# Kernel optimization log

Hardware: AMD Instinct MI355X
Metric: run time of the kernel (lower is better)

The kernel has to match this reference:

```python
import jax, jax.numpy as jnp
import numpy as np

KS = 3
PAD = 1
N = KS * KS  # 9 sampling points


def setup_inputs() -> dict:
    key = jax.random.key(0)
    k1, k2, k3 = jax.random.split(key, 3)
    B, C, H, W = 8, 64, 96, 96
    OUT = 64
    x = jax.random.normal(k1, (B, C, H, W), jnp.float32)
    offset = jax.random.normal(k2, (B, 2 * N, H, W), jnp.float32)
    conv_w = jax.random.normal(k3, (OUT, C * N, KS, KS), jnp.float32) * 0.02
    conv_b = jnp.zeros((OUT,), jnp.float32)
    return {"x": x, "offset": offset, "conv_w": conv_w, "conv_b": conv_b}


def _deform_gather(x, offset):
    # zero-pad spatially (nn.ZeroPad2d)
    xp = jnp.pad(x, ((0, 0), (0, 0), (PAD, PAD), (PAD, PAD)))
    b, c, h, w = xp.shape
    _, _, ho, wo = offset.shape
    # base kernel grid (row, col) pairs, shape (N, 2)
    grid = jnp.stack(
        jnp.meshgrid(jnp.arange(KS), jnp.arange(KS), indexing='ij'), axis=-1
    ).reshape(-1, 2).astype(offset.dtype)
    # offsets: (b, 2N, ho, wo) -> (b, ho, wo, N, 2)
    off = offset.transpose(0, 2, 3, 1).reshape(b, ho, wo, N, 2)
    p = grid[None, None, None] + off                       # (b, ho, wo, N, 2)
    # replicate torch's non-contiguous permute+reshape exactly (row-major)
    p = p.transpose(0, 3, 1, 2, 4).reshape(b, 2 * N, ho, wo)
    qx = jnp.clip(p[:, :N], 0, w - 1)                      # (b, N, ho, wo)
    qy = jnp.clip(p[:, N:], 0, h - 1)
    x0 = jnp.clip(jnp.floor(qx).astype(jnp.int32), 0, w - 1)
    x1 = jnp.clip(x0 + 1, 0, w - 1)
    y0 = jnp.clip(jnp.floor(qy).astype(jnp.int32), 0, h - 1)
    y1 = jnp.clip(y0 + 1, 0, h - 1)
    xf = xp.reshape(b, c, h * w)

    def g(iy, ix):
        idx = (iy * w + ix).reshape(b, 1, -1)              # (b, 1, N*ho*wo)
        v = jnp.take_along_axis(
            xf, jnp.broadcast_to(idx, (b, c, idx.shape[-1])), axis=2)
        return v.reshape(b, c, N, ho, wo)

    v00 = g(y0, x0); v01 = g(y0, x1); v10 = g(y1, x0); v11 = g(y1, x1)
    wx = (qx - x0.astype(qx.dtype))[:, None]               # (b, 1, N, ho, wo)
    wy = (qy - y0.astype(qy.dtype))[:, None]
    val = (v00 * (1 - wx) + v01 * wx) * (1 - wy) + (v10 * (1 - wx) + v11 * wx) * wy
    # (b, c, N, ho, wo) -> (b, c, ho, wo, N) -> (b, c*N, ho, wo)
    return val.transpose(0, 1, 3, 4, 2).reshape(b, c * N, ho, wo)


def reference(x, offset, conv_w, conv_b):
    xo = _deform_gather(x, offset)
    out = jax.lax.conv_general_dilated(
        xo, conv_w, window_strides=(1, 1), padding='VALID',
        dimension_numbers=('NCHW', 'OIHW', 'NCHW'))
    return out + conv_b[None, :, None, None]
```

## Files before the change

kernel.cpp:

```cpp
#include <hip/hip_runtime.h>

typedef short bf16x8 __attribute__((ext_vector_type(8)));
typedef float f32x4  __attribute__((ext_vector_type(4)));
typedef float f32x16 __attribute__((ext_vector_type(16)));

#define Sx 9216
#define ROWW 96
#define WB_USHORTS 331776
#define OW 94
#define XO_USHORTS ((size_t)8 * 96 * ROWW * 576)
#define XT_OFF_BYTES (2 * (size_t)WB_USHORTS + 2 * XO_USHORTS)
#define NEED_NEW (XT_OFF_BYTES + (size_t)8 * Sx * 64 * 4)
#define NOUT 4524032

__device__ __forceinline__ unsigned short bf16r(float f) {
    unsigned int u = __float_as_uint(f);
    u += 0x7fffu + ((u >> 16) & 1u);
    return (unsigned short)(u >> 16);
}

__device__ __forceinline__ void gload16(const void* g, void* l) {
    __builtin_amdgcn_global_load_lds(
        (const __attribute__((address_space(1))) void*)g,
        (__attribute__((address_space(3))) void*)l, 16, 0, 0);
}

__global__ __launch_bounds__(256)
void wprep32_k(const float* __restrict__ w, unsigned short* __restrict__ Wb) {
    int id = blockIdx.x * 256 + threadIdx.x;
    if (id >= 648 * 64) return;
    int lane = id & 63;
    int fm   = id >> 6;
    int m    = fm & 1;
    int rest = fm >> 1;
    int k16  = rest & 3;
    int rest2= rest >> 2;
    int qc   = rest2 / 9;
    int t    = rest2 - qc * 9;
    int o    = m * 32 + (lane & 31);
    int cb   = k16 * 16 + (lane >> 5) * 8;
    unsigned short v[8];
    #pragma unroll
    for (int j = 0; j < 8; ++j)
        v[j] = bf16r(w[(size_t)o * 5184 + ((cb + j) * 9 + qc) * 9 + t]);
    uint4 u;
    u.x = v[0] | ((unsigned)v[1] << 16);
    u.y = v[2] | ((unsigned)v[3] << 16);
    u.z = v[4] | ((unsigned)v[5] << 16);
    u.w = v[6] | ((unsigned)v[7] << 16);
    *(uint4*)(Wb + (size_t)id * 8) = u;
}

__global__ __launch_bounds__(256)
void wprep_k(const float* __restrict__ w, unsigned short* __restrict__ Wb) {
    int id = blockIdx.x * 256 + threadIdx.x;
    if (id >= 162 * 4 * 64) return;
    int lane = id & 63;
    int fm   = id >> 6;
    int mt   = fm & 3;
    int step = fm >> 2;
    int qc   = step / 18;
    int rs   = step - qc * 18;
    int t    = rs >> 1;
    int q32  = rs & 1;
    int o    = mt * 16 + (lane & 15);
    int cib  = q32 * 32 + (lane >> 4) * 8;
    unsigned short v[8];
    #pragma unroll
    for (int j = 0; j < 8; ++j) {
        int qorig = (cib + j) * 9 + qc;
        v[j] = bf16r(w[(size_t)o * 5184 + qorig * 9 + t]);
    }
    uint4 u;
    u.x = v[0] | ((unsigned)v[1] << 16);
    u.y = v[2] | ((unsigned)v[3] << 16);
    u.z = v[4] | ((unsigned)v[5] << 16);
    u.w = v[6] | ((unsigned)v[7] << 16);
    *(uint4*)(Wb + (size_t)id * 8) = u;
}

__global__ __launch_bounds__(256)
void xt_k(const float* __restrict__ x, float* __restrict__ xt) {
    __shared__ float t[64][65];
    const int tid = threadIdx.x;
    const int r2b = blockIdx.x * 64;
    const int b   = blockIdx.y;
    const int qq  = tid >> 6;
    const int ll  = tid & 63;
    #pragma unroll
    for (int cc = 0; cc < 16; ++cc) {
        int ci = cc * 4 + qq;
        t[ci][ll] = x[((size_t)(b * 64 + ci)) * Sx + r2b + ll];
    }
    __syncthreads();
    #pragma unroll
    for (int rr = 0; rr < 16; ++rr) {
        int r2l = rr * 4 + qq;
        xt[((size_t)b * Sx + r2b + r2l) * 64 + ll] = t[ll][r2l];
    }
}

__device__ __forceinline__ void decode_phase1(
        const float* __restrict__ ob, int x0b, int y,
        int (*sA)[288], float (*sW)[288], int tid) {
    for (int e = tid; e < 288; e += 256) {
        int chr = e >> 5;
        int xl  = e & 31;
        int r2  = y * 96 + x0b + xl;
        int n   = r2 % 9;
        int r   = chr * 1024 + r2 / 9;
        float q2[2];
        #pragma unroll
        for (int c2 = 0; c2 < 2; ++c2) {
            int k    = n + 9 * c2;
            int f    = k * Sx + r;
            int nn   = f / 18432;
            int t    = f - nn * 18432;
            int comp = t & 1;
            int pos  = t >> 1;
            int nd3  = nn / 3;
            float gg = comp ? (float)(nn - nd3 * 3) : (float)nd3;
            q2[c2] = gg + ob[(size_t)(2 * nn + comp) * Sx + pos];
        }
        float qx = fminf(fmaxf(q2[0], 0.f), 97.f);
        float qy = fminf(fmaxf(q2[1], 0.f), 97.f);
        int x0 = (int)qx; if (x0 > 97) x0 = 97;
        int y0 = (int)qy; if (y0 > 97) y0 = 97;
        float fx = qx - (float)x0;
        float fy = qy - (float)y0;
        int x1 = x0 + 1; if (x1 > 97) x1 = 97;
        int y1 = y0 + 1; if (y1 > 97) y1 = 97;
        int ix0 = x0 - 1, ix1 = x1 - 1, iy0 = y0 - 1, iy1 = y1 - 1;
        float vx0 = (ix0 >= 0 && ix0 < 96) ? 1.f : 0.f;
        float vx1 = (ix1 >= 0 && ix1 < 96) ? 1.f : 0.f;
        float vy0 = (iy0 >= 0 && iy0 < 96) ? 1.f : 0.f;
        float vy1 = (iy1 >= 0 && iy1 < 96) ? 1.f : 0.f;
        int cx0 = min(max(ix0, 0), 95), cx1 = min(max(ix1, 0), 95);
        int cy0 = min(max(iy0, 0), 95), cy1 = min(max(iy1, 0), 95);
        sW[0][e] = (1.f - fx) * (1.f - fy) * vx0 * vy0;
        sW[1][e] = fx * (1.f - fy) * vx1 * vy0;
        sW[2][e] = (1.f - fx) * fy * vx0 * vy1;
        sW[3][e] = fx * fy * vx1 * vy1;
        sA[0][e] = cy0 * 96 + cx0;
        sA[1][e] = cy0 * 96 + cx1;
        sA[2][e] = cy1 * 96 + cx0;
        sA[3][e] = cy1 * 96 + cx1;
    }
}

__global__ __launch_bounds__(256, 4)
void gather_xt(const float* __restrict__ xt, const float* __restrict__ off,
               unsigned short* __restrict__ xo) {
    __shared__ int   sA[4][288];
    __shared__ float sW[4][288];
    const int tid = threadIdx.x;
    const int x0b = blockIdx.x * 32;
    const int y   = blockIdx.y;
    const int b   = blockIdx.z;
    decode_phase1(off + (size_t)b * 18 * Sx, x0b, y, sA, sW, tid);
    __syncthreads();

    const int lane = tid & 63;
    const int wv   = tid >> 6;
    const float* xtb = xt + (size_t)b * Sx * 64 + lane;
    unsigned short* xob =
        xo + ((size_t)(b * 96 + y) * ROWW + x0b) * 576 + lane;

    #pragma unroll 4
    for (int i = 0; i < 72; ++i) {
        int e   = wv * 72 + i;
        int chr = e >> 5;
        int xl  = e & 31;
        float v = sW[0][e] * xtb[(size_t)sA[0][e] * 64]
                + sW[1][e] * xtb[(size_t)sA[1][e] * 64]
                + sW[2][e] * xtb[(size_t)sA[2][e] * 64]
                + sW[3][e] * xtb[(size_t)sA[3][e] * 64];
        xob[xl * 576 + chr * 64] = bf16r(v);
    }
}

__global__ __launch_bounds__(256, 2)
void gather_fb(const float* __restrict__ x, const float* __restrict__ off,
               unsigned short* __restrict__ xo) {
    __shared__ int   sA[4][288];
    __shared__ float sW[4][288];
    const int tid = threadIdx.x;
    const int x0b = blockIdx.x * 32;
    const int y   = blockIdx.y;
    const int b   = blockIdx.z;
    decode_phase1(off + (size_t)b * 18 * Sx, x0b, y, sA, sW, tid);
    __syncthreads();

    const int xl = tid & 31;
    const int g  = tid >> 5;
    const float* xb = x + (size_t)b * 64 * Sx + (size_t)g * 8 * Sx;
    uint4* dst = (uint4*)(xo + ((size_t)(b * 96 + y) * ROWW + (x0b + xl)) * 576) + g;

    #pragma unroll
    for (int chr = 0; chr < 9; ++chr) {
        int e = chr * 32 + xl;
        int   a00 = sA[0][e], a01 = sA[1][e], a10 = sA[2][e], a11 = sA[3][e];
        float w00 = sW[0][e], w01 = sW[1][e], w10 = sW[2][e], w11 = sW[3][e];
        unsigned short v[8];
        #pragma unroll
        for (int i = 0; i < 8; ++i) {
            const float* xc = xb + (size_t)i * Sx;
            v[i] = bf16r(w00 * xc[a00] + w01 * xc[a01]
                       + w10 * xc[a10] + w11 * xc[a11]);
        }
        uint4 u;
        u.x = v[0] | ((unsigned)v[1] << 16);
        u.y = v[2] | ((unsigned)v[3] << 16);
        u.z = v[4] | ((unsigned)v[5] << 16);
        u.w = v[6] | ((unsigned)v[7] << 16);
        dst[chr * 8] = u;
    }
}

__global__ __launch_bounds__(192, 2)
void conv32_k(const unsigned short* __restrict__ xo,
              const unsigned short* __restrict__ Wb,
              const float* __restrict__ bias,
              float* __restrict__ out, float* __restrict__ pbuf) {
    const int lane = threadIdx.x & 63;
    const int wn   = threadIdx.x >> 6;
    const int lin  = blockIdx.x;
    const int b    = lin & 7;
    const int rest = lin >> 3;
    const int ks   = rest & 1;
    const int p    = rest >> 1;

    __shared__ unsigned short tile[4 * 6656];
    const char* tb = (const char*)tile;

    f32x16 acc[2][2];
    #pragma unroll
    for (int m = 0; m < 2; ++m)
        #pragma unroll
        for (int ro = 0; ro < 2; ++ro)
            acc[m][ro] = (f32x16){0.f,0.f,0.f,0.f,0.f,0.f,0.f,0.f,
                                  0.f,0.f,0.f,0.f,0.f,0.f,0.f,0.f};

    const bf16x8* W8 = (const bf16x8*)Wb;
    const int xl  = lane >> 3;
    const int sl  = lane & 7;
    const int swz = (sl ^ xl) * 8;
    const size_t rowbase = (size_t)(b * 96 + 2 * p) * (ROWW * 576);

    const int qc0 = ks ? 5 : 0;
    const int qc1 = ks ? 9 : 5;

    for (int qc = qc0; qc < qc1; ++qc) {
        if (qc > qc0) __syncthreads();
        #pragma unroll
        for (int i = 0; i < 18; ++i) {
            int idx = wn + 3 * i;
            if (idx < 52) {
                int row = idx / 13;
                int xi  = idx - row * 13;
                gload16(xo + rowbase + (size_t)row * (ROWW * 576)
                           + (size_t)(xi * 8 + xl) * 576 + qc * 64 + swz,
                        tile + row * 6656 + xi * 512);
            }
        }
        asm volatile("s_waitcnt vmcnt(0)" ::: "memory");
        __syncthreads();

        #pragma unroll
        for (int st = 0; st < 36; ++st) {
            const int t = st >> 2, k16 = st & 3;
            const int ky = t / 3, kx = t - (t / 3) * 3;
            const int fb2 = ((qc * 9 + t) * 4 + k16) * 2;
            bf16x8 a0 = W8[(fb2 + 0) * 64 + lane];
            bf16x8 a1 = W8[(fb2 + 1) * 64 + lane];
            const int xpix = wn * 32 + (lane & 31) + kx;
            const int slot = (k16 * 2 + (lane >> 5)) ^ (xpix & 7);
            bf16x8 b0 = *(const bf16x8*)(tb + (0 + ky) * 13312 + xpix * 128 + slot * 16);
            bf16x8 b1 = *(const bf16x8*)(tb + (1 + ky) * 13312 + xpix * 128 + slot * 16);
            __builtin_amdgcn_s_setprio(1);
            acc[0][0] = __builtin_amdgcn_mfma_f32_32x32x16_bf16(a0, b0, acc[0][0], 0, 0, 0);
            acc[0][1] = __builtin_amdgcn_mfma_f32_32x32x16_bf16(a0, b1, acc[0][1], 0, 0, 0);
            acc[1][0] = __builtin_amdgcn_mfma_f32_32x32x16_bf16(a1, b0, acc[1][0], 0, 0, 0);
            acc[1][1] = __builtin_amdgcn_mfma_f32_32x32x16_bf16(a1, b1, acc[1][1], 0, 0, 0);
            __builtin_amdgcn_s_setprio(0);
        }
    }

    const int ox = wn * 32 + (lane & 31);
    float* dst = ks ? pbuf : out;
    if (ox < OW) {
        #pragma unroll
        for (int m = 0; m < 2; ++m) {
            #pragma unroll
            for (int ro = 0; ro < 2; ++ro) {
                const int oyr = 2 * p + ro;
                #pragma unroll
                for (int reg = 0; reg < 16; ++reg) {
                    int row = (reg & 3) + 8 * (reg >> 2) + 4 * (lane >> 5);
                    int o = m * 32 + row;
                    float v = acc[m][ro][reg];
                    if (!ks) v += bias[o];
                    dst[(((size_t)b * 64 + o) * OW + oyr) * OW + ox] = v;
                }
            }
        }
    }
}

__global__ __launch_bounds__(256)
void reduce_k(float* __restrict__ out, const float* __restrict__ pbuf) {
    const size_t N4 = NOUT / 4;
    for (size_t i = blockIdx.x * 256 + threadIdx.x; i < N4;
         i += (size_t)gridDim.x * 256) {
        float4 a = ((const float4*)out)[i];
        float4 c = ((const float4*)pbuf)[i];
        a.x += c.x; a.y += c.y; a.z += c.z; a.w += c.w;
        ((float4*)out)[i] = a;
    }
}

__global__ __launch_bounds__(192, 3)
void conv_fb(const unsigned short* __restrict__ xo,
             const unsigned short* __restrict__ Wb,
             const float* __restrict__ bias,
             float* __restrict__ out) {
    const int lane = threadIdx.x & 63;
    const int wn   = threadIdx.x >> 6;
    const int lin  = blockIdx.x;
    const int b    = lin & 7;
    const int rest = lin >> 3;
    const int mh   = rest & 1;
    const int p    = rest >> 1;

    __shared__ unsigned short tile[4 * 6144 + 256];
    char* tb = (char*)tile;

    f32x4 acc[2][2][2];
    #pragma unroll
    for (int m = 0; m < 2; ++m)
        #pragma unroll
        for (int ro = 0; ro < 2; ++ro)
            #pragma unroll
            for (int xf = 0; xf < 2; ++xf)
                acc[m][ro][xf] = (f32x4){0.f, 0.f, 0.f, 0.f};

    const bf16x8* W8 = (const bf16x8*)Wb;
    const int xl  = lane >> 3;
    const int sl  = lane & 7;
    const int swz = (sl ^ xl) * 8;
    const size_t rowbase = (size_t)(b * 96 + 2 * p) * (ROWW * 576);

    for (int qc = 0; qc < 9; ++qc) {
        if (qc) __syncthreads();
        #pragma unroll
        for (int i = 0; i < 16; ++i) {
            int j   = wn * 16 + i;
            int row = j / 12;
            int xi  = j - row * 12;
            gload16(xo + rowbase + (size_t)row * (ROWW * 576)
                       + (size_t)(xi * 8 + xl) * 576 + qc * 64 + swz,
                    tile + row * 6144 + xi * 512);
        }
        asm volatile("s_waitcnt vmcnt(0)" ::: "memory");
        __syncthreads();

        #pragma unroll
        for (int st = 0; st < 18; ++st) {
            const int t = st >> 1, q32 = st & 1;
            const int ky = t / 3, kx = t - (t / 3) * 3;
            const int step = qc * 18 + st;
            bf16x8 a0 = W8[(step * 4 + mh * 2 + 0) * 64 + lane];
            bf16x8 a1 = W8[(step * 4 + mh * 2 + 1) * 64 + lane];
            bf16x8 bf[2][2];
            #pragma unroll
            for (int ro = 0; ro < 2; ++ro) {
                #pragma unroll
                for (int xf = 0; xf < 2; ++xf) {
                    int xpix = wn * 32 + xf * 16 + (lane & 15) + kx;
                    int slot = (q32 * 4 + (lane >> 4)) ^ (xpix & 7);
                    bf[ro][xf] = *(const bf16x8*)(tb + (ro + ky) * 12288
                                                    + xpix * 128 + slot * 16);
                }
            }
            #pragma unroll
            for (int ro = 0; ro < 2; ++ro) {
                #pragma unroll
                for (int xf = 0; xf < 2; ++xf) {
                    acc[0][ro][xf] = __builtin_amdgcn_mfma_f32_16x16x32_bf16(a0, bf[ro][xf], acc[0][ro][xf], 0, 0, 0);
                    acc[1][ro][xf] = __builtin_amdgcn_mfma_f32_16x16x32_bf16(a1, bf[ro][xf], acc[1][ro][xf], 0, 0, 0);
                }
            }
        }
    }

    #pragma unroll
    for (int m = 0; m < 2; ++m) {
        #pragma unroll
        for (int ro = 0; ro < 2; ++ro) {
            #pragma unroll
            for (int xf = 0; xf < 2; ++xf) {
                int ox = wn * 32 + xf * 16 + (lane & 15);
                if (ox < OW) {
                    int oyr = 2 * p + ro;
                    #pragma unroll
                    for (int j = 0; j < 4; ++j) {
                        int o = mh * 32 + m * 16 + (lane >> 4) * 4 + j;
                        out[(((size_t)b * 64 + o) * OW + oyr) * OW + ox] =
                            acc[m][ro][xf][j] + bias[o];
                    }
                }
            }
        }
    }
}

extern "C" void kernel_launch(void* const* d_in, const int* in_sizes, int n_in,
                              void* d_out, int out_size, void* d_ws, size_t ws_size,
                              hipStream_t stream) {
    const float* x    = (const float*)d_in[0];
    const float* off  = (const float*)d_in[1];
    const float* w    = (const float*)d_in[2];
    const float* bias = (const float*)d_in[3];
    unsigned short* ws16 = (unsigned short*)d_ws;
    unsigned short* Wb   = ws16;
    unsigned short* xo   = ws16 + WB_USHORTS;

    if (ws_size >= NEED_NEW) {
        float* xt = (float*)((char*)d_ws + XT_OFF_BYTES);
        wprep32_k<<<162, 256, 0, stream>>>(w, Wb);
        xt_k<<<dim3(144, 8), 256, 0, stream>>>(x, xt);
        gather_xt<<<dim3(3, 96, 8), 256, 0, stream>>>(xt, off, xo);
        float* pbuf = xt;
        conv32_k<<<752, 192, 0, stream>>>(xo, Wb, bias, (float*)d_out, pbuf);
        reduce_k<<<2048, 256, 0, stream>>>((float*)d_out, pbuf);
    } else {
        wprep_k<<<162, 256, 0, stream>>>(w, Wb);
        gather_fb<<<dim3(3, 96, 8), 256, 0, stream>>>(x, off, xo);
        conv_fb<<<752, 192, 0, stream>>>(xo, Wb, bias, (float*)d_out);
    }
}
```

Before: 143.9 us.

## Stage conv weights in LDS with double buffering and switch to 16x16x32 MFMA

```diff
diff --git a/kernel.cpp b/kernel.cpp
--- a/kernel.cpp
+++ b/kernel.cpp
@@ -2,7 +2,6 @@
 
 typedef short bf16x8 __attribute__((ext_vector_type(8)));
 typedef float f32x4  __attribute__((ext_vector_type(4)));
-typedef float f32x16 __attribute__((ext_vector_type(16)));
 
 #define Sx 9216
 #define ROWW 96
@@ -23,32 +22,6 @@
     __builtin_amdgcn_global_load_lds(
         (const __attribute__((address_space(1))) void*)g,
         (__attribute__((address_space(3))) void*)l, 16, 0, 0);
-}
-
-__global__ __launch_bounds__(256)
-void wprep32_k(const float* __restrict__ w, unsigned short* __restrict__ Wb) {
-    int id = blockIdx.x * 256 + threadIdx.x;
-    if (id >= 648 * 64) return;
-    int lane = id & 63;
-    int fm   = id >> 6;
-    int m    = fm & 1;
-    int rest = fm >> 1;
-    int k16  = rest & 3;
-    int rest2= rest >> 2;
-    int qc   = rest2 / 9;
-    int t    = rest2 - qc * 9;
-    int o    = m * 32 + (lane & 31);
-    int cb   = k16 * 16 + (lane >> 5) * 8;
-    unsigned short v[8];
-    #pragma unroll
-    for (int j = 0; j < 8; ++j)
-        v[j] = bf16r(w[(size_t)o * 5184 + ((cb + j) * 9 + qc) * 9 + t]);
-    uint4 u;
-    u.x = v[0] | ((unsigned)v[1] << 16);
-    u.y = v[2] | ((unsigned)v[3] << 16);
-    u.z = v[4] | ((unsigned)v[5] << 16);
-    u.w = v[6] | ((unsigned)v[7] << 16);
-    *(uint4*)(Wb + (size_t)id * 8) = u;
 }
 
 __global__ __launch_bounds__(256)
@@ -218,30 +191,30 @@
 }
 
 __global__ __launch_bounds__(192, 2)
-void conv32_k(const unsigned short* __restrict__ xo,
-              const unsigned short* __restrict__ Wb,
-              const float* __restrict__ bias,
-              float* __restrict__ out, float* __restrict__ pbuf) {
+void conv_sk(const unsigned short* __restrict__ xo,
+             const unsigned short* __restrict__ Wb,
+             const float* __restrict__ bias,
+             float* __restrict__ out, float* __restrict__ pbuf) {
     const int lane = threadIdx.x & 63;
     const int wn   = threadIdx.x >> 6;
     const int lin  = blockIdx.x;
     const int b    = lin & 7;
-    const int rest = lin >> 3;
-    const int ks   = rest & 1;
-    const int p    = rest >> 1;
-
-    __shared__ unsigned short tile[4 * 6656];
-    const char* tb = (const char*)tile;
-
-    f32x16 acc[2][2];
-    #pragma unroll
-    for (int m = 0; m < 2; ++m)
+    const int ks   = (lin >> 3) & 1;
+    const int p    = lin >> 4;
+
+    __shared__ unsigned short tileB[4 * 6144 + 128];
+    __shared__ unsigned short tileA[2 * 6144];
+    char* tb = (char*)tileB;
+
+    f32x4 acc[4][2][2];
+    #pragma unroll
+    for (int m = 0; m < 4; ++m)
         #pragma unroll
         for (int ro = 0; ro < 2; ++ro)
-            acc[m][ro] = (f32x16){0.f,0.f,0.f,0.f,0.f,0.f,0.f,0.f,
-                                  0.f,0.f,0.f,0.f,0.f,0.f,0.f,0.f};
-
-    const bf16x8* W8 = (const bf16x8*)Wb;
+            #pragma unroll
+            for (int xf = 0; xf < 2; ++xf)
+                acc[m][ro][xf] = (f32x4){0.f, 0.f, 0.f, 0.f};
+
     const int xl  = lane >> 3;
     const int sl  = lane & 7;
     const int swz = (sl ^ xl) * 8;
@@ -251,56 +224,93 @@
     const int qc1 = ks ? 9 : 5;
 
     for (int qc = qc0; qc < qc1; ++qc) {
-        if (qc > qc0) __syncthreads();
-        #pragma unroll
-        for (int i = 0; i < 18; ++i) {
-            int idx = wn + 3 * i;
-            if (idx < 52) {
-                int row = idx / 13;
-                int xi  = idx - row * 13;
-                gload16(xo + rowbase + (size_t)row * (ROWW * 576)
-                           + (size_t)(xi * 8 + xl) * 576 + qc * 64 + swz,
-                        tile + row * 6656 + xi * 512);
+        #pragma unroll
+        for (int i = 0; i < 16; ++i) {
+            int j   = wn * 16 + i;
+            int row = j / 12;
+            int xi  = j - row * 12;
+            gload16(xo + rowbase + (size_t)row * (ROWW * 576)
+                       + (size_t)(xi * 8 + xl) * 576 + qc * 64 + swz,
+                    tileB + row * 6144 + xi * 512);
+        }
+        {
+            const int fb = qc * 18 * 4;
+            #pragma unroll
+            for (int k = 0; k < 4; ++k) {
+                int f = wn * 4 + k;
+                gload16(Wb + (size_t)(fb + f) * 512 + lane * 8, tileA + f * 512);
             }
         }
         asm volatile("s_waitcnt vmcnt(0)" ::: "memory");
         __syncthreads();
 
         #pragma unroll
-        for (int st = 0; st < 36; ++st) {
-            const int t = st >> 2, k16 = st & 3;
-            const int ky = t / 3, kx = t - (t / 3) * 3;
-            const int fb2 = ((qc * 9 + t) * 4 + k16) * 2;
-            bf16x8 a0 = W8[(fb2 + 0) * 64 + lane];
-            bf16x8 a1 = W8[(fb2 + 1) * 64 + lane];
-            const int xpix = wn * 32 + (lane & 31) + kx;
-            const int slot = (k16 * 2 + (lane >> 5)) ^ (xpix & 7);
-            bf16x8 b0 = *(const bf16x8*)(tb + (0 + ky) * 13312 + xpix * 128 + slot * 16);
-            bf16x8 b1 = *(const bf16x8*)(tb + (1 + ky) * 13312 + xpix * 128 + slot * 16);
-            __builtin_amdgcn_s_setprio(1);
-            acc[0][0] = __builtin_amdgcn_mfma_f32_32x32x16_bf16(a0, b0, acc[0][0], 0, 0, 0);
-            acc[0][1] = __builtin_amdgcn_mfma_f32_32x32x16_bf16(a0, b1, acc[0][1], 0, 0, 0);
-            acc[1][0] = __builtin_amdgcn_mfma_f32_32x32x16_bf16(a1, b0, acc[1][0], 0, 0, 0);
-            acc[1][1] = __builtin_amdgcn_mfma_f32_32x32x16_bf16(a1, b1, acc[1][1], 0, 0, 0);
-            __builtin_amdgcn_s_setprio(0);
-        }
-    }
-
-    const int ox = wn * 32 + (lane & 31);
+        for (int c = 0; c < 6; ++c) {
+            if (c < 5) {
+                const int fb = (qc * 18 + (c + 1) * 3) * 4;
+                #pragma unroll
+                for (int k = 0; k < 4; ++k) {
+                    int f = wn * 4 + k;
+                    gload16(Wb + (size_t)(fb + f) * 512 + lane * 8,
+                            tileA + ((c + 1) & 1) * 6144 + f * 512);
+                }
+            }
+            const unsigned short* ab = tileA + (c & 1) * 6144;
+            #pragma unroll
+            for (int ls = 0; ls < 3; ++ls) {
+                const int st = c * 3 + ls;
+                const int t = st >> 1, q32 = st & 1;
+                const int ky = t / 3, kx = t - (t / 3) * 3;
+                bf16x8 a0 = *((const bf16x8*)(ab + (ls * 4 + 0) * 512) + lane);
+                bf16x8 a1 = *((const bf16x8*)(ab + (ls * 4 + 1) * 512) + lane);
+                bf16x8 a2 = *((const bf16x8*)(ab + (ls * 4 + 2) * 512) + lane);
+                bf16x8 a3 = *((const bf16x8*)(ab + (ls * 4 + 3) * 512) + lane);
+                bf16x8 bf[2][2];
+                #pragma unroll
+                for (int ro = 0; ro < 2; ++ro) {
+                    #pragma unroll
+                    for (int xf = 0; xf < 2; ++xf) {
+                        int xpix = wn * 32 + xf * 16 + (lane & 15) + kx;
+                        int slot = (q32 * 4 + (lane >> 4)) ^ (xpix & 7);
+                        bf[ro][xf] = *(const bf16x8*)(tb + (ro + ky) * 12288
+                                                        + xpix * 128 + slot * 16);
+                    }
+                }
+                __builtin_amdgcn_s_setprio(1);
+                #pragma unroll
+                for (int ro = 0; ro < 2; ++ro) {
+                    #pragma unroll
+                    for (int xf = 0; xf < 2; ++xf) {
+                        acc[0][ro][xf] = __builtin_amdgcn_mfma_f32_16x16x32_bf16(a0, bf[ro][xf], acc[0][ro][xf], 0, 0, 0);
+                        acc[1][ro][xf] = __builtin_amdgcn_mfma_f32_16x16x32_bf16(a1, bf[ro][xf], acc[1][ro][xf], 0, 0, 0);
+                        acc[2][ro][xf] = __builtin_amdgcn_mfma_f32_16x16x32_bf16(a2, bf[ro][xf], acc[2][ro][xf], 0, 0, 0);
+                        acc[3][ro][xf] = __builtin_amdgcn_mfma_f32_16x16x32_bf16(a3, bf[ro][xf], acc[3][ro][xf], 0, 0, 0);
+                    }
+                }
+                __builtin_amdgcn_s_setprio(0);
+            }
+            asm volatile("s_waitcnt vmcnt(0)" ::: "memory");
+            __syncthreads();
+        }
+    }
+
     float* dst = ks ? pbuf : out;
-    if (ox < OW) {
-        #pragma unroll
-        for (int m = 0; m < 2; ++m) {
-            #pragma unroll
-            for (int ro = 0; ro < 2; ++ro) {
-                const int oyr = 2 * p + ro;
-                #pragma unroll
-                for (int reg = 0; reg < 16; ++reg) {
-                    int row = (reg & 3) + 8 * (reg >> 2) + 4 * (lane >> 5);
-                    int o = m * 32 + row;
-                    float v = acc[m][ro][reg];
-                    if (!ks) v += bias[o];
-                    dst[(((size_t)b * 64 + o) * OW + oyr) * OW + ox] = v;
+    #pragma unroll
+    for (int m = 0; m < 4; ++m) {
+        #pragma unroll
+        for (int ro = 0; ro < 2; ++ro) {
+            #pragma unroll
+            for (int xf = 0; xf < 2; ++xf) {
+                int ox = wn * 32 + xf * 16 + (lane & 15);
+                if (ox < OW) {
+                    int oyr = 2 * p + ro;
+                    #pragma unroll
+                    for (int j = 0; j < 4; ++j) {
+                        int o = m * 16 + (lane >> 4) * 4 + j;
+                        float v = acc[m][ro][xf][j];
+                        if (!ks) v += bias[o];
+                        dst[(((size_t)b * 64 + o) * OW + oyr) * OW + ox] = v;
+                    }
                 }
             }
         }
@@ -425,16 +435,15 @@
     unsigned short* Wb   = ws16;
     unsigned short* xo   = ws16 + WB_USHORTS;
 
+    wprep_k<<<162, 256, 0, stream>>>(w, Wb);
     if (ws_size >= NEED_NEW) {
         float* xt = (float*)((char*)d_ws + XT_OFF_BYTES);
-        wprep32_k<<<162, 256, 0, stream>>>(w, Wb);
         xt_k<<<dim3(144, 8), 256, 0, stream>>>(x, xt);
         gather_xt<<<dim3(3, 96, 8), 256, 0, stream>>>(xt, off, xo);
         float* pbuf = xt;
-        conv32_k<<<752, 192, 0, stream>>>(xo, Wb, bias, (float*)d_out, pbuf);
+        conv_sk<<<752, 192, 0, stream>>>(xo, Wb, bias, (float*)d_out, pbuf);
         reduce_k<<<2048, 256, 0, stream>>>((float*)d_out, pbuf);
     } else {
-        wprep_k<<<162, 256, 0, stream>>>(w, Wb);
         gather_fb<<<dim3(3, 96, 8), 256, 0, stream>>>(x, off, xo);
         conv_fb<<<752, 192, 0, stream>>>(xo, Wb, bias, (float*)d_out);
     }
```

New measurement: 156.5 us. 1.09x slower.
